# Kernel tuning notes

Measured on AMD Instinct MI355X. Metric: run time of the kernel, lower is better.

The kernel has to match this reference:

```python
import jax, jax.numpy as jnp
import numpy as np

THRESHOLD = 0.05
STRIDE = (1, 1)
PADDING = ((1, 1), (1, 1))


def ternary_quantize(w, threshold=THRESHOLD):
    # w -> {-1, 0, +1}; zero where |w| <= threshold
    mask = (jnp.abs(w) > threshold).astype(w.dtype)
    return jnp.sign(w) * mask


def setup_inputs() -> dict:
    key = jax.random.key(0)
    k1, k2 = jax.random.split(key)
    B, Cin, H, W = 32, 256, 56, 56
    Cout, kH, kW = 256, 3, 3
    fan_in = Cin * kH * kW
    std = np.sqrt(2.0 / fan_in) * 2.0
    x = jax.random.normal(k1, (B, Cin, H, W), dtype=jnp.float32)
    weight = jax.random.normal(k2, (Cout, Cin, kH, kW), dtype=jnp.float32) * std
    bias = jnp.zeros((Cout,), dtype=jnp.float32)
    return {"x": x, "weight": weight, "bias": bias}


def reference(x, weight, bias):
    w_t = ternary_quantize(weight, THRESHOLD)
    out = jax.lax.conv_general_dilated(
        x, w_t,
        window_strides=STRIDE,
        padding=PADDING,
        dimension_numbers=("NCHW", "OIHW", "NCHW"),
    )
    return out + bias[None, :, None, None]
```

## Files before the change

### kernel.cpp

```cpp
#include <hip/hip_runtime.h>

#define CIN   256
#define COUT  256
#define HH    56
#define WW    56
#define BATCH 32
#define KTOT  2304
#define HP    58
#define WP    58
#define NPIX  (BATCH*HH*WW)
#define HWSZ  (HH*WW)
#define BN    224
#define NBLK  (NPIX/BN)

typedef __bf16 bf16x8 __attribute__((ext_vector_type(8)));
typedef float  f32x4  __attribute__((ext_vector_type(4)));

#define AS1 __attribute__((address_space(1)))
#define AS3 __attribute__((address_space(3)))

__device__ __forceinline__ unsigned short f2bf(float f) {
  union { float f; unsigned int u; } v; v.f = f;
  unsigned int u = v.u;
  u += 0x7fffu + ((u >> 16) & 1u);
  return (unsigned short)(u >> 16);
}

__device__ __forceinline__ void async16(const void* g, void* l) {
  __builtin_amdgcn_global_load_lds((const AS1 unsigned int*)g,
                                   (AS3 unsigned int*)l, 16, 0, 0);
}

#define TSTR 60
#define QBLKS 2304
__global__ __launch_bounds__(256) void prep(const float* __restrict__ w,
                                            unsigned short* __restrict__ wr,
                                            const float* __restrict__ x,
                                            unsigned short* __restrict__ xp) {
  const int bx = blockIdx.x;
  if (bx < QBLKS) {
    int tid = bx * 256 + threadIdx.x;
    int co  = tid / KTOT;
    int rem = tid - co * KTOT;
    int tap = rem >> 8;
    int ci  = rem & 255;
    int kh  = tap / 3;
    int kw  = tap - kh * 3;
    float v = w[((co * CIN + ci) * 3 + kh) * 3 + kw];
    float q = (fabsf(v) > 0.05f) ? ((v > 0.f) ? 1.f : -1.f) : 0.f;
    wr[tid] = f2bf(q);
    return;
  }
  const int pbx = bx - QBLKS;
  const int nhp = pbx >> 2;
  const int n   = nhp / HP;
  const int hp  = nhp - n * HP;
  const int ci0 = (pbx & 3) << 6;
  const int t   = threadIdx.x;
  const size_t obase = (size_t)nhp * (WP * 256);

  __shared__ __align__(16) float tile[64 * TSTR];
  const bool hborder = (hp == 0) || (hp == HP - 1);

  if (!hborder) {
    const int h = hp - 1;
    #pragma unroll
    for (int it = 0; it < 4; ++it) {
      int linear = it * 256 + t;
      if (linear < 896) {
        int cil = linear / 14;
        int w4  = linear - cil * 14;
        *(float4*)&tile[cil * TSTR + w4 * 4] =
            *(const float4*)&x[(((size_t)(n * CIN + ci0 + cil)) * HH + h) * WW + w4 * 4];
      }
    }
  }
  __syncthreads();

  #pragma unroll
  for (int it = 0; it < 2; ++it) {
    int linear = it * 256 + t;
    if (linear < 464) {
      int wp = linear >> 3;
      int g  = linear & 7;
      unsigned int pk[4] = {0u, 0u, 0u, 0u};
      if (!hborder && wp != 0 && wp != WP - 1) {
        #pragma unroll
        for (int j = 0; j < 4; ++j) {
          int jr = (j + g) & 3;
          unsigned int lo = f2bf(tile[(g * 8 + 2 * jr) * TSTR + (wp - 1)]);
          unsigned int hi = f2bf(tile[(g * 8 + 2 * jr + 1) * TSTR + (wp - 1)]);
          pk[jr] = lo | (hi << 16);
        }
      }
      uint4 v; v.x = pk[0]; v.y = pk[1]; v.z = pk[2]; v.w = pk[3];
      *(uint4*)(xp + obase + (size_t)wp * 256 + ci0 + g * 8) = v;
    }
  }
}


#define NOWAIT (void)0
#define VM4 asm volatile("s_waitcnt vmcnt(4)" ::: "memory")
#define VM0 asm volatile("s_waitcnt vmcnt(0)" ::: "memory")

#define STAGE4(buf_, kn_) do {                                                \
  const int kn__ = (kn_);                                                     \
  const size_t koW_ = (size_t)kn__ << 5;                                      \
  const int tap_ = kn__ >> 3;                                                 \
  const int kh_  = tap_ / 3;                                                  \
  const int kw_  = tap_ - kh_ * 3;                                            \
  const size_t koX_ = (size_t)((kh_ * WP + kw_) * 256 + ((kn__ & 7) << 5));   \
  char* da_ = smem + (buf_) * 32768 + t * 16;                                 \
  char* db_ = smem + (buf_) * 32768 + 16384 + t * 16;                         \
  async16(Wr + koW_ + aSrc0, da_);                                            \
  async16(Wr + koW_ + aSrc1, da_ + 8192);                                     \
  async16(Xp + koX_ + bSrc0, db_);                                            \
  async16(Xp + koX_ + bSrc1, db_ + 8192);                                     \
} while (0)

#define PHASE(bc_, bn_, cur_, nxt_, DOBF_, WAITE, ...) do {                   \
  __VA_ARGS__;                                                                \
  bf16x8 af_[4];                                                              \
  _Pragma("unroll")                                                           \
  for (int mt = 0; mt < 4; ++mt)                                              \
    af_[mt] = *(const bf16x8*)(smem + (bc_) * 32768 + rdA + mt * 1024);       \
  if (DOBF_) {                                                                \
    _Pragma("unroll")                                                         \
    for (int nt = 0; nt < 7; ++nt)                                            \
      nxt_[nt] = *(const bf16x8*)(smem + (bn_) * 32768 + 16384 + rdB + nt * 1024);\
  }                                                                           \
  _Pragma("unroll")                                                           \
  for (int mt = 0; mt < 4; ++mt)                                              \
    _Pragma("unroll")                                                         \
    for (int nt = 0; nt < 7; ++nt)                                            \
      acc[mt][nt] = __builtin_amdgcn_mfma_f32_16x16x32_bf16(                  \
          af_[mt], cur_[nt], acc[mt][nt], 0, 0, 0);                           \
  WAITE;                                                                      \
  __builtin_amdgcn_s_barrier();                                               \
  __builtin_amdgcn_sched_barrier(0);                                          \
} while (0)

__global__ __launch_bounds__(512, 2) void conv_gemm(
    const unsigned short* __restrict__ Wr,
    const unsigned short* __restrict__ Xp,
    const float* __restrict__ bias,
    float* __restrict__ out) {
  extern __shared__ char smem[];

  const int t    = threadIdx.x;
  const int lane = t & 63;
  const int wv   = t >> 6;
  const int wm   = wv >> 1;
  const int wn   = wv & 1;
  const int l15  = lane & 15;
  const int quad = lane >> 4;

  const int bid = blockIdx.x;
  const int pb  = (bid & 7) * 56 + (bid >> 3);
  const int p0  = pb * BN;

  const int srow = t >> 2;
  const int schk = (t & 3) ^ ((srow >> 1) & 3);

  const size_t aSrc0 = (size_t)srow * KTOT + schk * 8;
  const size_t aSrc1 = aSrc0 + (size_t)128 * KTOT;

  const int pA = p0 + srow;
  const int pB = pA + 128;
  const int nA = pA / HWSZ;  const int hwA = pA - nA * HWSZ;
  const int hA = hwA / WW;   const int wA  = hwA - hA * WW;
  const int nB = pB / HWSZ;  const int hwB = pB - nB * HWSZ;
  const int hB = hwB / WW;   const int wB  = hwB - hB * WW;
  const size_t bSrc0 = ((size_t)((nA * HP + hA) * WP + wA)) * 256 + schk * 8;
  const size_t bSrc1 = ((size_t)((nB * HP + hB) * WP + wB)) * 256 + schk * 8;

  const int rchk = (quad ^ ((l15 >> 1) & 3)) * 16;
  const int rdA  = (wm * 64  + l15) * 64 + rchk;
  const int rdB  = (wn * 112 + l15) * 64 + rchk;

  f32x4 acc[4][7];
  #pragma unroll
  for (int i = 0; i < 4; ++i)
    #pragma unroll
    for (int j = 0; j < 7; ++j)
      acc[i][j] = (f32x4){0.f, 0.f, 0.f, 0.f};

  bf16x8 bfA[7], bfB[7];

  STAGE4(0, 0);
  STAGE4(1, 1);
  STAGE4(2, 2);
  VM4;
  __builtin_amdgcn_s_barrier();
  __builtin_amdgcn_sched_barrier(0);
  #pragma unroll
  for (int nt = 0; nt < 7; ++nt)
    bfA[nt] = *(const bf16x8*)(smem + 16384 + rdB + nt * 1024);

  #pragma unroll 1
  for (int it = 0; it < 17; ++it) {
    const int k0 = 4 * it;
    PHASE(0, 1, bfA, bfB, 1, VM4, STAGE4(3, k0 + 3));
    PHASE(1, 2, bfB, bfA, 1, VM4, STAGE4(0, k0 + 4));
    PHASE(2, 3, bfA, bfB, 1, VM4, STAGE4(1, k0 + 5));
    PHASE(3, 0, bfB, bfA, 1, VM4, STAGE4(2, k0 + 6));
  }
  PHASE(0, 1, bfA, bfB, 1, VM4, STAGE4(3, 71));
  PHASE(1, 2, bfB, bfA, 1, VM0, NOWAIT);
  PHASE(2, 3, bfA, bfB, 1, NOWAIT, NOWAIT);
  PHASE(3, 0, bfB, bfA, 0, NOWAIT, NOWAIT);

  float bv[4][4];
  #pragma unroll
  for (int mt = 0; mt < 4; ++mt)
    #pragma unroll
    for (int r = 0; r < 4; ++r)
      bv[mt][r] = bias[wm * 64 + mt * 16 + quad * 4 + r];

  #pragma unroll
  for (int nt = 0; nt < 7; ++nt) {
    const int p  = p0 + wn * 112 + nt * 16 + l15;
    const int np = p / HWSZ;
    const int hw = p - np * HWSZ;
    const size_t obase = (size_t)np * (COUT * HWSZ) + hw;
    #pragma unroll
    for (int mt = 0; mt < 4; ++mt) {
      const int co = wm * 64 + mt * 16 + quad * 4;
      #pragma unroll
      for (int r = 0; r < 4; ++r)
        out[obase + (size_t)(co + r) * HWSZ] = acc[mt][nt][r] + bv[mt][r];
    }
  }
}

extern "C" void kernel_launch(void* const* d_in, const int* in_sizes, int n_in,
                              void* d_out, int out_size, void* d_ws, size_t ws_size,
                              hipStream_t stream) {
  const float* x    = (const float*)d_in[0];
  const float* w    = (const float*)d_in[1];
  const float* bias = (const float*)d_in[2];
  float* out        = (float*)d_out;

  unsigned short* xp = (unsigned short*)d_ws;
  unsigned short* wr = (unsigned short*)((char*)d_ws + 55115776);

  prep<<<dim3(QBLKS + BATCH * HP * 4), dim3(256), 0, stream>>>(w, wr, x, xp);

  (void)hipFuncSetAttribute((const void*)conv_gemm,
                            hipFuncAttributeMaxDynamicSharedMemorySize, 131072);
  conv_gemm<<<dim3(NBLK), dim3(512), 131072, stream>>>(wr, xp, bias, out);
}
```

Baseline: 307.5 us.

## Restructure prep kernel: coalesced weight quantization via LDS and full-row transpose

Weight quantization now gives each block two output channels and reads them contiguously, staging the transposed bf16 result in shared memory so it can be written out with 16-byte stores. The input pad/transpose now gives each block a whole padded row across all 256 channels. It converts to bf16 before staging, using a rotated (swizzled) LDS layout with vector reads. This replaces strided scalar weight reads and narrow channel-group blocks, cutting block count and global transaction overhead. The GEMM kernel is unchanged, so only the prep portion of the total time is affected.

```diff
diff --git a/kernel.cpp b/kernel.cpp
--- a/kernel.cpp
+++ b/kernel.cpp
@@ -31,70 +31,69 @@
                                    (AS3 unsigned int*)l, 16, 0, 0);
 }
 
-#define TSTR 60
-#define QBLKS 2304
-__global__ __launch_bounds__(256) void prep(const float* __restrict__ w,
+__global__ __launch_bounds__(512) void prep(const float* __restrict__ w,
                                             unsigned short* __restrict__ wr,
                                             const float* __restrict__ x,
                                             unsigned short* __restrict__ xp) {
+  __shared__ __align__(16) unsigned short sh[56 * 256];
   const int bx = blockIdx.x;
-  if (bx < QBLKS) {
-    int tid = bx * 256 + threadIdx.x;
-    int co  = tid / KTOT;
-    int rem = tid - co * KTOT;
-    int tap = rem >> 8;
-    int ci  = rem & 255;
-    int kh  = tap / 3;
-    int kw  = tap - kh * 3;
-    float v = w[((co * CIN + ci) * 3 + kh) * 3 + kw];
-    float q = (fabsf(v) > 0.05f) ? ((v > 0.f) ? 1.f : -1.f) : 0.f;
-    wr[tid] = f2bf(q);
+  const int t  = threadIdx.x;
+
+  if (bx < 128) {
+    const int ci  = t & 255;
+    const int sub = t >> 8;
+    const int co  = bx * 2 + sub;
+    const float* ws = w + (size_t)co * 2304 + ci * 9;
+    unsigned short* qs = sh + sub * 2304;
+    #pragma unroll
+    for (int j = 0; j < 9; ++j) {
+      float v = ws[j];
+      float q = (fabsf(v) > 0.05f) ? ((v > 0.f) ? 1.f : -1.f) : 0.f;
+      qs[j * 256 + ci] = f2bf(q);
+    }
+    __syncthreads();
+    uint4* dst = (uint4*)(wr + (size_t)bx * 2 * 2304);
+    const uint4* src = (const uint4*)sh;
+    dst[t] = src[t];
+    if (t < 64) dst[512 + t] = src[512 + t];
     return;
   }
-  const int pbx = bx - QBLKS;
-  const int nhp = pbx >> 2;
-  const int n   = nhp / HP;
-  const int hp  = nhp - n * HP;
-  const int ci0 = (pbx & 3) << 6;
-  const int t   = threadIdx.x;
-  const size_t obase = (size_t)nhp * (WP * 256);
-
-  __shared__ __align__(16) float tile[64 * TSTR];
-  const bool hborder = (hp == 0) || (hp == HP - 1);
-
-  if (!hborder) {
+
+  const int pbx = bx - 128;
+  const int n   = pbx / HP;
+  const int hp  = pbx - n * HP;
+  const size_t obase = (size_t)(n * HP + hp) * (WP * 256);
+  const bool hb = (hp == 0) || (hp == HP - 1);
+
+  if (!hb) {
     const int h = hp - 1;
     #pragma unroll
-    for (int it = 0; it < 4; ++it) {
-      int linear = it * 256 + t;
-      if (linear < 896) {
-        int cil = linear / 14;
-        int w4  = linear - cil * 14;
-        *(float4*)&tile[cil * TSTR + w4 * 4] =
-            *(const float4*)&x[(((size_t)(n * CIN + ci0 + cil)) * HH + h) * WW + w4 * 4];
+    for (int it = 0; it < 7; ++it) {
+      int lin = it * 512 + t;
+      int ci  = lin / 14;
+      int w4  = lin - ci * 14;
+      float4 v = *(const float4*)&x[((size_t)(n * CIN + ci) * HH + h) * WW + w4 * 4];
+      #pragma unroll
+      for (int k = 0; k < 4; ++k) {
+        int wdx = w4 * 4 + k;
+        sh[wdx * 256 + ((ci + 8 * wdx) & 255)] = f2bf(((const float*)&v)[k]);
       }
     }
   }
   __syncthreads();
 
   #pragma unroll
-  for (int it = 0; it < 2; ++it) {
-    int linear = it * 256 + t;
-    if (linear < 464) {
-      int wp = linear >> 3;
-      int g  = linear & 7;
-      unsigned int pk[4] = {0u, 0u, 0u, 0u};
-      if (!hborder && wp != 0 && wp != WP - 1) {
-        #pragma unroll
-        for (int j = 0; j < 4; ++j) {
-          int jr = (j + g) & 3;
-          unsigned int lo = f2bf(tile[(g * 8 + 2 * jr) * TSTR + (wp - 1)]);
-          unsigned int hi = f2bf(tile[(g * 8 + 2 * jr + 1) * TSTR + (wp - 1)]);
-          pk[jr] = lo | (hi << 16);
-        }
+  for (int it = 0; it < 4; ++it) {
+    int lin = it * 512 + t;
+    if (lin < 1856) {
+      int wp = lin >> 5;
+      int g2 = lin & 31;
+      uint4 v = {0u, 0u, 0u, 0u};
+      if (!hb && wp != 0 && wp != WP - 1) {
+        int wdx = wp - 1;
+        v = *(const uint4*)&sh[wdx * 256 + ((g2 * 8 + 8 * wdx) & 255)];
       }
-      uint4 v; v.x = pk[0]; v.y = pk[1]; v.z = pk[2]; v.w = pk[3];
-      *(uint4*)(xp + obase + (size_t)wp * 256 + ci0 + g * 8) = v;
+      *(uint4*)(xp + obase + (size_t)wp * 256 + g2 * 8) = v;
     }
   }
 }
@@ -245,7 +244,7 @@
   unsigned short* xp = (unsigned short*)d_ws;
   unsigned short* wr = (unsigned short*)((char*)d_ws + 55115776);
 
-  prep<<<dim3(QBLKS + BATCH * HP * 4), dim3(256), 0, stream>>>(w, wr, x, xp);
+  prep<<<dim3(128 + BATCH * HP), dim3(512), 0, stream>>>(w, wr, x, xp);
 
   (void)hipFuncSetAttribute((const void*)conv_gemm,
                             hipFuncAttributeMaxDynamicSharedMemorySize, 131072);
```

New measurement: 306.1 us. No clear change (-0.5%).
